# Kernel tuning notes

Hardware: AMD Instinct MI355X
Metric: run time of the kernel (lower is better)

The kernel has to match this reference:

```python
import jax, jax.numpy as jnp
import numpy as np

B, L, D, H = 8, 1024, 1024, 16
DH = D // H  # dim_per_head = 64
HG = H // 2  # global/local head split


def setup_inputs() -> dict:
    key = jax.random.key(0)
    ks = jax.random.split(key, 10)
    s = 1.0 / np.sqrt(D)
    return {
        "key": jax.random.normal(ks[0], (B, L, D), jnp.float32),
        "value": jax.random.normal(ks[1], (B, L, D), jnp.float32),
        "query": jax.random.normal(ks[2], (B, L, D), jnp.float32),
        "mask": jax.random.bernoulli(ks[3], 0.1, (B, L, L)),
        "additional_mask": jax.random.bernoulli(ks[4], 0.1, (B, L)),
        "Wk": jax.random.normal(ks[5], (D, D), jnp.float32) * s,
        "bk": jnp.zeros((D,), jnp.float32),
        "Wv": jax.random.normal(ks[6], (D, D), jnp.float32) * s,
        "bv": jnp.zeros((D,), jnp.float32),
        "Wq": jax.random.normal(ks[7], (D, D), jnp.float32) * s,
        "bq": jnp.zeros((D,), jnp.float32),
        "Wo": jax.random.normal(ks[8], (D, D), jnp.float32) * s,
        "bo": jnp.zeros((D,), jnp.float32),
    }


def _shape(x):
    # [B, L, D] -> [B, H, L, DH]
    return x.reshape(B, -1, H, DH).transpose(0, 2, 1, 3)


def reference(key, value, query, mask, additional_mask,
              Wk, bk, Wv, bv, Wq, bq, Wo, bo):
    # projections (torch Linear: x @ W.T + b)
    k = _shape(key @ Wk.T + bk)
    v = _shape(value @ Wv.T + bv)
    q = _shape(query @ Wq.T + bq) * (1.0 / np.sqrt(DH))  # scale query (edge_feature=None, additional_mask given)

    qg, ql = q[:, :HG], q[:, HG:]
    kg, kl = k[:, :HG], k[:, HG:]
    vg, vl = v[:, :HG], v[:, HG:]

    # global heads: standard masked attention
    score_g = jnp.einsum('bhqd,bhkd->bhqk', qg, kg)
    top_score = score_g[:, 0]  # taken BEFORE masking, as in original
    score_g = jnp.where(mask[:, None, :, :], -1e18, score_g)
    attn_g = jax.nn.softmax(score_g, axis=-1)  # dropout = identity (eval)
    ctx_g = jnp.einsum('bhqk,bhkd->bhqd', attn_g, vg)

    # local heads: additional_mask [B, k] broadcast over heads and queries
    score_l = jnp.einsum('bhqd,bhkd->bhqk', ql, kl)
    score_l = jnp.where(additional_mask[:, None, None, :], -1e18, score_l)
    attn_l = jax.nn.softmax(score_l, axis=-1)
    ctx_l = jnp.einsum('bhqk,bhkd->bhqd', attn_l, vl)

    ctx = jnp.concatenate([ctx_g, ctx_l], axis=1)          # [B, H, L, DH]
    ctx = ctx.transpose(0, 2, 1, 3).reshape(B, -1, D)      # unshape -> [B, L, D]
    out = ctx @ Wo.T + bo
    return out, top_score
```

## Files before the change

kernel.cpp:

```cpp
#include <hip/hip_runtime.h>
#include <hip/hip_bf16.h>

typedef unsigned short u16;
typedef unsigned int u32;
typedef __attribute__((ext_vector_type(8))) short short8;
typedef __attribute__((ext_vector_type(4))) short short4v;
typedef __attribute__((ext_vector_type(4))) float floatx4;

#define BB 8
#define LL 1024
#define DD 1024
#define HH 16
#define DHH 64
#define NEGBIG (-3.0e38f)
#define QSCALE 0.1803368801111204f
#define LN2F   0.6931471805599453f
#define DEFER_THR 12.0f

__device__ inline u16 f2b(float f) {
  union { __hip_bfloat16 h; u16 u; } cv;
  cv.h = __float2bfloat16(f);
  return cv.u;
}
__device__ inline float b2f(u16 u) {
  union { u16 u; __hip_bfloat16 h; } cv;
  cv.u = u;
  return __bfloat162float(cv.h);
}
__device__ inline float fin(float v, float sentinel) {
  return (fabsf(v) < 1e30f) ? v : sentinel;
}
__device__ inline float fexp2(float x) {
#if __has_builtin(__builtin_amdgcn_exp2f)
  return __builtin_amdgcn_exp2f(x);
#else
  return exp2f(x);
#endif
}
__device__ inline void async16(const void* g, void* l) {
  __builtin_amdgcn_global_load_lds(
      (__attribute__((address_space(1))) void*)(const_cast<void*>(g)),
      (__attribute__((address_space(3))) void*)l, 16, 0, 0);
}


__global__ __launch_bounds__(256) void convpack(
    const float* __restrict__ Wk, const float* __restrict__ Wv,
    const float* __restrict__ Wq, const float* __restrict__ Wo,
    const int* __restrict__ mask, const int* __restrict__ amask,
    u16* __restrict__ Wkb, u16* __restrict__ Wvb, u16* __restrict__ Wqb,
    u16* __restrict__ Wob, u32* __restrict__ maskb, u32* __restrict__ amaskb) {
  const int job = blockIdx.y;
  const int gtid = blockIdx.x * 256 + threadIdx.x;
  const int stride = gridDim.x * 256;

  if (job < 4) {
    const float* src; u16* dst;
    switch (job) {
      case 0: src = Wk; dst = Wkb; break;
      case 1: src = Wv; dst = Wvb; break;
      case 2: src = Wq; dst = Wqb; break;
      default: src = Wo; dst = Wob; break;
    }
    const size_t n4 = (size_t)DD * DD / 4;
    for (size_t i = gtid; i < n4; i += stride) {
      float4 v = ((const float4*)src)[i];
      short4v s;
      s[0] = (short)f2b(v.x); s[1] = (short)f2b(v.y);
      s[2] = (short)f2b(v.z); s[3] = (short)f2b(v.w);
      *(short4v*)(dst + i * 4) = s;
    }
  } else if (job == 4) {
    const size_t nw = (size_t)BB * LL * LL / 32;
    for (size_t w = gtid; w < nw; w += stride) {
      const int4* src = (const int4*)(mask + w * 32);
      u32 bits = 0;
#pragma unroll
      for (int c = 0; c < 8; c++) {
        int4 v = src[c];
        bits |= (u32)(v.x != 0) << (c * 4);
        bits |= (u32)(v.y != 0) << (c * 4 + 1);
        bits |= (u32)(v.z != 0) << (c * 4 + 2);
        bits |= (u32)(v.w != 0) << (c * 4 + 3);
      }
      maskb[w] = bits;
    }
  } else {
    const int nw = BB * LL / 32;
    for (int w = gtid; w < nw; w += stride) {
      const int4* src = (const int4*)(amask + w * 32);
      u32 bits = 0;
#pragma unroll
      for (int c = 0; c < 8; c++) {
        int4 v = src[c];
        bits |= (u32)(v.x != 0) << (c * 4);
        bits |= (u32)(v.y != 0) << (c * 4 + 1);
        bits |= (u32)(v.z != 0) << (c * 4 + 2);
        bits |= (u32)(v.w != 0) << (c * 4 + 3);
      }
      amaskb[w] = bits;
    }
  }
}

__global__ __launch_bounds__(256) void gemm_qkv(
    const float* __restrict__ key, const float* __restrict__ value,
    const float* __restrict__ query, const u16* __restrict__ Wkb,
    const u16* __restrict__ Wvb, const u16* __restrict__ Wqb,
    const float* __restrict__ bk, const float* __restrict__ bv,
    const float* __restrict__ bq, u16* __restrict__ kbuf,
    u16* __restrict__ vbt, u16* __restrict__ qbuf) {
  __shared__ u16 As[2][128 * 32];
  __shared__ u16 Ws[2][128 * 32];

  const int z = blockIdx.z;
  const int tid = threadIdx.x;
  const int wave = tid >> 6, lane = tid & 63;
  const int lr = lane & 15, lq = lane >> 4;
  const int row0 = blockIdx.x * 128;
  const int col0 = blockIdx.y * 128;
  const int wm = (wave & 1) * 64, wn = (wave >> 1) * 64;

  floatx4 acc[4][4];
#pragma unroll
  for (int i = 0; i < 4; i++)
#pragma unroll
    for (int j = 0; j < 4; j++) acc[i][j] = (floatx4){0.f, 0.f, 0.f, 0.f};

  const float* A = (z == 0) ? key : (z == 1) ? value : query;
  const u16* Wb  = (z == 0) ? Wkb : (z == 1) ? Wvb : Wqb;

  const int cc0 = tid, cc1 = 256 + tid;
  const u16* Wg0 = Wb + (size_t)(col0 + (cc0 >> 2)) * 1024 + (cc0 & 3) * 8;
  const u16* Wg1 = Wb + (size_t)(col0 + (cc1 >> 2)) * 1024 + (cc1 & 3) * 8;

  auto stageW = [&](int t, int buf) {
    const int o = t * 32;
    async16(Wg0 + o, &Ws[buf][wave * 512]);
    async16(Wg1 + o, &Ws[buf][2048 + wave * 512]);
  };
  auto loadA = [&](int t, float4* ag) {
#pragma unroll
    for (int it = 0; it < 4; it++) {
      const int cc = it * 256 + tid;
      ag[it] = *(const float4*)(A + (size_t)(row0 + (cc >> 3)) * 1024 +
                                (cc & 7) * 4 + t * 32);
    }
  };
  auto writeA = [&](int buf, const float4* ag) {
#pragma unroll
    for (int it = 0; it < 4; it++) {
      const int cc = it * 256 + tid;
      short4v s;
      s[0] = (short)f2b(ag[it].x); s[1] = (short)f2b(ag[it].y);
      s[2] = (short)f2b(ag[it].z); s[3] = (short)f2b(ag[it].w);
      *(short4v*)(&As[buf][(cc >> 3) * 32 + (cc & 7) * 4]) = s;
    }
  };

  {
    float4 ag0[4];
    loadA(0, ag0);
    stageW(0, 0);
    writeA(0, ag0);
  }

  for (int t = 0; t < 32; t++) {
    const int buf = t & 1;
    __syncthreads();
    float4 ag[4];
    if (t < 31) {
      stageW(t + 1, buf ^ 1);
      loadA(t + 1, ag);
    }

    short8 af[4], wf[4];
#pragma unroll
    for (int mi = 0; mi < 4; mi++)
      af[mi] = *(const short8*)(&As[buf][(wm + mi * 16 + lr) * 32 + lq * 8]);
#pragma unroll
    for (int ni = 0; ni < 4; ni++)
      wf[ni] = *(const short8*)(&Ws[buf][(wn + ni * 16 + lr) * 32 + lq * 8]);
#pragma unroll
    for (int mi = 0; mi < 4; mi++)
#pragma unroll
      for (int ni = 0; ni < 4; ni++)
        acc[mi][ni] = __builtin_amdgcn_mfma_f32_16x16x32_bf16(af[mi], wf[ni],
                                                              acc[mi][ni], 0, 0, 0);

    if (t < 31) writeA(buf ^ 1, ag);
  }

  const float scale = (z == 2) ? QSCALE : 1.0f;
  const float* bias = (z == 0) ? bk : (z == 1) ? bv : bq;
  u16* outb = (z == 0) ? kbuf : qbuf;

#pragma unroll
  for (int ni = 0; ni < 4; ni++) {
    const int col = col0 + wn + ni * 16 + lr;
    const float bvv = bias[col];
#pragma unroll
    for (int mi = 0; mi < 4; mi++) {
#pragma unroll
      for (int r = 0; r < 4; r++) {
        const int row = row0 + wm + mi * 16 + lq * 4 + r;
        const float v = (acc[mi][ni][r] + bvv) * scale;
        const int b = row >> 10, l = row & 1023, h = col >> 6, dh = col & 63;
        if (z == 1)
          vbt[((b * HH + h) * DHH + dh) * LL + l] = f2b(v);
        else
          outb[((b * HH + h) * LL + l) * DHH + dh] = f2b(v);
      }
    }
  }
}

template <int OUT>
__global__ __launch_bounds__(256) void gemm_b(
    const u16* __restrict__ A, const u16* __restrict__ Wb,
    const float* __restrict__ bias, void* __restrict__ outv, float scale) {
  __shared__ u16 As[128 * 32];
  __shared__ u16 Ws[128 * 32];

  const int tid = threadIdx.x;
  const int wave = tid >> 6, lane = tid & 63;
  const int lr = lane & 15, lq = lane >> 4;
  const int row0 = blockIdx.x * 128;
  const int col0 = blockIdx.y * 128;
  const int wm = (wave & 1) * 64, wn = (wave >> 1) * 64;

  floatx4 acc[4][4];
#pragma unroll
  for (int i = 0; i < 4; i++)
#pragma unroll
    for (int j = 0; j < 4; j++) acc[i][j] = (floatx4){0.f, 0.f, 0.f, 0.f};

  const int cc0 = tid, cc1 = 256 + tid;
  const u16* Ag0 = A + (size_t)(row0 + (cc0 >> 2)) * 1024 + (cc0 & 3) * 8;
  const u16* Ag1 = A + (size_t)(row0 + (cc1 >> 2)) * 1024 + (cc1 & 3) * 8;
  const u16* Wg0 = Wb + (size_t)(col0 + (cc0 >> 2)) * 1024 + (cc0 & 3) * 8;
  const u16* Wg1 = Wb + (size_t)(col0 + (cc1 >> 2)) * 1024 + (cc1 & 3) * 8;
  u16* As0 = As + wave * 512;
  u16* As1 = As + 2048 + wave * 512;
  u16* Ws0 = Ws + wave * 512;
  u16* Ws1 = Ws + 2048 + wave * 512;

  for (int k0 = 0; k0 < 1024; k0 += 32) {
    __syncthreads();
    async16(Ag0 + k0, As0);
    async16(Ag1 + k0, As1);
    async16(Wg0 + k0, Ws0);
    async16(Wg1 + k0, Ws1);
    __syncthreads();

    short8 af[4], wf[4];
#pragma unroll
    for (int mi = 0; mi < 4; mi++)
      af[mi] = *(const short8*)(As + (wm + mi * 16 + lr) * 32 + lq * 8);
#pragma unroll
    for (int ni = 0; ni < 4; ni++)
      wf[ni] = *(const short8*)(Ws + (wn + ni * 16 + lr) * 32 + lq * 8);
#pragma unroll
    for (int mi = 0; mi < 4; mi++)
#pragma unroll
      for (int ni = 0; ni < 4; ni++)
        acc[mi][ni] = __builtin_amdgcn_mfma_f32_16x16x32_bf16(af[mi], wf[ni],
                                                              acc[mi][ni], 0, 0, 0);
  }

#pragma unroll
  for (int ni = 0; ni < 4; ni++) {
    const int col = col0 + wn + ni * 16 + lr;
    const float bv = bias[col];
#pragma unroll
    for (int mi = 0; mi < 4; mi++) {
#pragma unroll
      for (int r = 0; r < 4; r++) {
        const int row = row0 + wm + mi * 16 + lq * 4 + r;
        const float v = (acc[mi][ni][r] + bv) * scale;
        if (OUT == 0) {
          const int b = row >> 10, l = row & 1023, h = col >> 6, dh = col & 63;
          ((u16*)outv)[((b * HH + h) * LL + l) * DHH + dh] = f2b(v);
        } else if (OUT == 2) {
          const int b = row >> 10, l = row & 1023, h = col >> 6, dh = col & 63;
          ((u16*)outv)[((b * HH + h) * DHH + dh) * LL + l] = f2b(v);
        } else {
          ((float*)outv)[(size_t)row * 1024 + col] = v;
        }
      }
    }
  }
}

__global__ __launch_bounds__(256) void attn_fast(
    const u16* __restrict__ qbuf, const u16* __restrict__ kbuf,
    const u16* __restrict__ vbt, const u32* __restrict__ maskb,
    const u32* __restrict__ amaskb, u16* __restrict__ ctx,
    float* __restrict__ top) {
  __shared__ u16 Ks[2][64 * 64];
  __shared__ u16 Vts[2][64 * 64];

  const int id = blockIdx.x;
  const int xcd = id & 7;
  const int r_ = id >> 3;
  const int b = r_ & 7;
  const int h = (((r_ >> 3) & 1) << 3) | (xcd ^ b);
  const int qt = r_ >> 4;

  const int tid = threadIdx.x, wave = tid >> 6, lane = tid & 63;
  const int lr = lane & 15, lq = lane >> 4;
  const int lq4 = lq * 4;
  const int x7 = lr & 7;

  const u16* Qg = qbuf + (size_t)((b * HH + h) * LL + qt * 128) * DHH;
  const u16* Kg = kbuf + (size_t)((b * HH + h) * LL) * DHH;
  const u16* Vtg = vbt + (size_t)((b * HH + h) * DHH) * LL;

  short8 qf[2][2];
#pragma unroll
  for (int mi = 0; mi < 2; mi++)
#pragma unroll
    for (int kk = 0; kk < 2; kk++)
      qf[mi][kk] = *(const short8*)(Qg + (wave * 32 + mi * 16 + lr) * 64 +
                                    kk * 32 + lq * 8);

  const int g0 = tid, g1 = 256 + tid;
  const int kr0 = g0 >> 3, kc0 = (g0 & 7) ^ (kr0 & 7);
  const int kr1 = g1 >> 3, kc1 = (g1 & 7) ^ (kr1 & 7);
  const int cs0 = ((0 + lq) ^ x7) * 8;
  const int cs1 = ((4 + lq) ^ x7) * 8;
  const int lqh = lq >> 1, lqb = (lq & 1) * 4;
  const int go00 = ((0 + lqh) ^ x7) * 8 + lqb;
  const int go01 = ((2 + lqh) ^ x7) * 8 + lqb;
  const int go10 = ((4 + lqh) ^ x7) * 8 + lqb;
  const int go11 = ((6 + lqh) ^ x7) * 8 + lqb;

  auto stage = [&](int kc, int buf) {
    async16(Kg + kc * 4096 + kr0 * 64 + kc0 * 8, &Ks[buf][wave * 512]);
    async16(Kg + kc * 4096 + kr1 * 64 + kc1 * 8, &Ks[buf][2048 + wave * 512]);
    async16(Vtg + (size_t)kr0 * LL + kc * 64 + kc0 * 8, &Vts[buf][wave * 512]);
    async16(Vtg + (size_t)kr1 * LL + kc * 64 + kc1 * 8,
            &Vts[buf][2048 + wave * 512]);
  };

  const int rowm0 = qt * 128 + wave * 32 + lr;
  const int rowm1 = rowm0 + 16;
  const u32* mb0 = (h < 8) ? maskb + (size_t)(b * LL + rowm0) * 32
                           : amaskb + b * 32;
  const u32* mb1 = (h < 8) ? maskb + (size_t)(b * LL + rowm1) * 32
                           : amaskb + b * 32;
  uint2 mwc0 = *(const uint2*)(mb0);
  uint2 mwc1 = *(const uint2*)(mb1);

  float mrow[2], lrow[2];
  floatx4 Oacc[2][4];
#pragma unroll
  for (int mi = 0; mi < 2; mi++) {
    mrow[mi] = NEGBIG;
    lrow[mi] = 0.f;
#pragma unroll
    for (int ni = 0; ni < 4; ni++) Oacc[mi][ni] = (floatx4){0.f, 0.f, 0.f, 0.f};
  }

  stage(0, 0);

  for (int kc = 0; kc < 16; kc++) {
    const int cur = kc & 1;
    __syncthreads();
    uint2 mwn0, mwn1;
    if (kc < 15) {
      stage(kc + 1, cur ^ 1);
      mwn0 = *(const uint2*)(mb0 + (kc + 1) * 2);
      mwn1 = *(const uint2*)(mb1 + (kc + 1) * 2);
    }
    const u16* Ksc = Ks[cur];
    const u16* Vtsc = Vts[cur];

    floatx4 S[2][4];
    __builtin_amdgcn_s_setprio(1);
#pragma unroll
    for (int nj = 0; nj < 4; nj++) {
      const short8 kf0 = *(const short8*)(Ksc + (nj * 16 + lr) * 64 + cs0);
      const short8 kf1 = *(const short8*)(Ksc + (nj * 16 + lr) * 64 + cs1);
#pragma unroll
      for (int mi = 0; mi < 2; mi++) {
        floatx4 z = (floatx4){0.f, 0.f, 0.f, 0.f};
        z = __builtin_amdgcn_mfma_f32_16x16x32_bf16(kf1, qf[mi][1], z, 0, 0, 0);
        z = __builtin_amdgcn_mfma_f32_16x16x32_bf16(kf0, qf[mi][0], z, 0, 0, 0);
        S[mi][nj] = z;
      }
    }
    __builtin_amdgcn_s_setprio(0);

    short8 pf[2][2];
#pragma unroll
    for (int mi = 0; mi < 2; mi++) {
      const int row = qt * 128 + wave * 32 + mi * 16 + lr;

      if (h == 0) {
        float* tp = top + (size_t)(b * LL + row) * LL + kc * 64 + lq4;
#pragma unroll
        for (int nj = 0; nj < 4; nj++) {
          float4 t;
          t.x = S[mi][nj][0] * LN2F; t.y = S[mi][nj][1] * LN2F;
          t.z = S[mi][nj][2] * LN2F; t.w = S[mi][nj][3] * LN2F;
          *(float4*)(tp + nj * 16) = t;
        }
      }

      {
        const uint2 mw = mi ? mwc1 : mwc0;
#pragma unroll
        for (int nj = 0; nj < 4; nj++) {
          const u32 nib = (((nj & 2) ? mw.y : mw.x) >> ((nj & 1) * 16 + lq4)) & 15u;
#pragma unroll
          for (int r = 0; r < 4; r++)
            if ((nib >> r) & 1) S[mi][nj][r] = -1e18f;
        }
      }

      float cm = fmaxf(fmaxf(S[mi][0][0], S[mi][0][1]),
                       fmaxf(S[mi][0][2], S[mi][0][3]));
#pragma unroll
      for (int nj = 1; nj < 4; nj++)
        cm = fmaxf(cm, fmaxf(fmaxf(S[mi][nj][0], S[mi][nj][1]),
                             fmaxf(S[mi][nj][2], S[mi][nj][3])));
      cm = fmaxf(cm, __shfl_xor(cm, 16, 64));
      cm = fmaxf(cm, __shfl_xor(cm, 32, 64));
      const float mold = mrow[mi];
      if (!__all(cm <= mold + DEFER_THR)) {
        const float mnew = fmaxf(mold, cm);
        const float alpha = fexp2(mold - mnew);
        mrow[mi] = mnew;
        lrow[mi] *= alpha;
#pragma unroll
        for (int ni = 0; ni < 4; ni++)
#pragma unroll
          for (int r = 0; r < 4; r++) Oacc[mi][ni][r] *= alpha;
      }
      const float mcur = mrow[mi];
      float rs = 0.f;
#pragma unroll
      for (int nj = 0; nj < 4; nj++)
#pragma unroll
        for (int r = 0; r < 4; r++) {
          const float p = fexp2(S[mi][nj][r] - mcur);
          S[mi][nj][r] = p;
          rs += p;
        }
      rs += __shfl_xor(rs, 16, 64);
      rs += __shfl_xor(rs, 32, 64);
      lrow[mi] += rs;

#pragma unroll
      for (int kk = 0; kk < 2; kk++) {
        short8 p;
#pragma unroll
        for (int r = 0; r < 4; r++) {
          p[r] = (short)f2b(S[mi][2 * kk][r]);
          p[4 + r] = (short)f2b(S[mi][2 * kk + 1][r]);
        }
        pf[mi][kk] = p;
      }
    }

    __builtin_amdgcn_s_setprio(1);
#pragma unroll
    for (int ni = 0; ni < 4; ni++) {
      const int rb = (ni * 16 + lr) * 64;
      const short4v v00 = *(const short4v*)(Vtsc + rb + go00);
      const short4v v01 = *(const short4v*)(Vtsc + rb + go01);
      const short4v v10 = *(const short4v*)(Vtsc + rb + go10);
      const short4v v11 = *(const short4v*)(Vtsc + rb + go11);
      const short8 vf0 = __builtin_shufflevector(v00, v01, 0, 1, 2, 3, 4, 5, 6, 7);
      const short8 vf1 = __builtin_shufflevector(v10, v11, 0, 1, 2, 3, 4, 5, 6, 7);
#pragma unroll
      for (int mi = 0; mi < 2; mi++) {
        Oacc[mi][ni] =
            __builtin_amdgcn_mfma_f32_16x16x32_bf16(vf0, pf[mi][0], Oacc[mi][ni], 0, 0, 0);
        Oacc[mi][ni] =
            __builtin_amdgcn_mfma_f32_16x16x32_bf16(vf1, pf[mi][1], Oacc[mi][ni], 0, 0, 0);
      }
    }
    __builtin_amdgcn_s_setprio(0);

    if (kc < 15) { mwc0 = mwn0; mwc1 = mwn1; }
  }

#pragma unroll
  for (int mi = 0; mi < 2; mi++) {
    const float inv = 1.0f / lrow[mi];
    const int row = qt * 128 + wave * 32 + mi * 16 + lr;
    u16* cp = ctx + (size_t)(b * LL + row) * DD + h * DHH + lq4;
#pragma unroll
    for (int ni = 0; ni < 4; ni++) {
      short4v o;
      o[0] = (short)f2b(Oacc[mi][ni][0] * inv);
      o[1] = (short)f2b(Oacc[mi][ni][1] * inv);
      o[2] = (short)f2b(Oacc[mi][ni][2] * inv);
      o[3] = (short)f2b(Oacc[mi][ni][3] * inv);
      *(short4v*)(cp + ni * 16) = o;
    }
  }
}

template <int MODE>
__global__ __launch_bounds__(256) void gemm_k(
    const void* __restrict__ Av, const float* __restrict__ W,
    const float* __restrict__ biasp, void* __restrict__ outv, float scale) {
  __shared__ u16 As[128 * 32];
  __shared__ u16 Ws[128 * 32];
  const int tid = threadIdx.x;
  const int wave = tid >> 6, lane = tid & 63;
  const int lr = lane & 15, lq = lane >> 4;
  const int row0 = blockIdx.x * 128;
  const int col0 = blockIdx.y * 128;
  const int wm = (wave & 1) * 64, wn = (wave >> 1) * 64;
  floatx4 acc[4][4];
#pragma unroll
  for (int i = 0; i < 4; i++)
#pragma unroll
    for (int j = 0; j < 4; j++) acc[i][j] = (floatx4){0.f, 0.f, 0.f, 0.f};
  const float* Af = (const float*)Av;
  const u16* Ab = (const u16*)Av;
  for (int k0 = 0; k0 < 1024; k0 += 32) {
    float4 wg[4];
#pragma unroll
    for (int it = 0; it < 4; it++) {
      const int cc = it * 256 + tid;
      wg[it] = *(const float4*)(W + (size_t)(col0 + (cc >> 3)) * 1024 + (cc & 7) * 4 + k0);
    }
    float4 ag[4];
    short8 ab0, ab1;
    if (MODE == 0) {
#pragma unroll
      for (int it = 0; it < 4; it++) {
        const int cc = it * 256 + tid;
        ag[it] = *(const float4*)(Af + (size_t)(row0 + (cc >> 3)) * 1024 + (cc & 7) * 4 + k0);
      }
    } else {
      const int cc0 = tid, cc1 = 256 + tid;
      ab0 = *(const short8*)(Ab + (size_t)(row0 + (cc0 >> 2)) * 1024 + (cc0 & 3) * 8 + k0);
      ab1 = *(const short8*)(Ab + (size_t)(row0 + (cc1 >> 2)) * 1024 + (cc1 & 3) * 8 + k0);
    }
    __syncthreads();
#pragma unroll
    for (int it = 0; it < 4; it++) {
      const int cc = it * 256 + tid;
      short4v s;
      s[0] = (short)f2b(wg[it].x); s[1] = (short)f2b(wg[it].y);
      s[2] = (short)f2b(wg[it].z); s[3] = (short)f2b(wg[it].w);
      *(short4v*)(Ws + (cc >> 3) * 32 + (cc & 7) * 4) = s;
    }
    if (MODE == 0) {
#pragma unroll
      for (int it = 0; it < 4; it++) {
        const int cc = it * 256 + tid;
        short4v s;
        s[0] = (short)f2b(ag[it].x); s[1] = (short)f2b(ag[it].y);
        s[2] = (short)f2b(ag[it].z); s[3] = (short)f2b(ag[it].w);
        *(short4v*)(As + (cc >> 3) * 32 + (cc & 7) * 4) = s;
      }
    } else {
      *(short8*)(As + tid * 8) = ab0;
      *(short8*)(As + (256 + tid) * 8) = ab1;
    }
    __syncthreads();
    short8 af[4], wf[4];
#pragma unroll
    for (int mi = 0; mi < 4; mi++)
      af[mi] = *(const short8*)(As + (wm + mi * 16 + lr) * 32 + lq * 8);
#pragma unroll
    for (int ni = 0; ni < 4; ni++)
      wf[ni] = *(const short8*)(Ws + (wn + ni * 16 + lr) * 32 + lq * 8);
#pragma unroll
    for (int mi = 0; mi < 4; mi++)
#pragma unroll
      for (int ni = 0; ni < 4; ni++)
        acc[mi][ni] = __builtin_amdgcn_mfma_f32_16x16x32_bf16(af[mi], wf[ni], acc[mi][ni], 0, 0, 0);
  }
#pragma unroll
  for (int ni = 0; ni < 4; ni++) {
    const int col = col0 + wn + ni * 16 + lr;
    const float bv = biasp[col];
#pragma unroll
    for (int mi = 0; mi < 4; mi++) {
#pragma unroll
      for (int r = 0; r < 4; r++) {
        const int row = row0 + wm + mi * 16 + lq * 4 + r;
        float v = (acc[mi][ni][r] + bv) * scale;
        v = fin(v, MODE == 0 ? 700.0f : 1000.0f);
        if (MODE == 0) {
          const int b = row >> 10, l = row & 1023, h = col >> 6, dh = col & 63;
          ((u16*)outv)[((b * HH + h) * LL + l) * DHH + dh] = f2b(v);
        } else {
          ((float*)outv)[(size_t)row * 1024 + col] = v;
        }
      }
    }
  }
}

__global__ __launch_bounds__(256) void attn_kernel(
    const u16* __restrict__ qbuf, const u16* __restrict__ kbuf,
    const u16* __restrict__ vbuf, const int* __restrict__ mask,
    const int* __restrict__ amask, u16* __restrict__ ctx,
    float* __restrict__ top) {
  __shared__ u16 Qs[128 * 64];
  __shared__ u16 Ks[64 * 64];
  __shared__ u16 Vts[64 * 64];
  __shared__ u16 Ps[4][32 * 64];
  const int qt = blockIdx.x, h = blockIdx.y, b = blockIdx.z;
  const int tid = threadIdx.x, wave = tid >> 6, lane = tid & 63;
  const int lr = lane & 15, lq = lane >> 4;
  const u16* Qg = qbuf + (size_t)((b * HH + h) * LL + qt * 128) * DHH;
  const u16* Kg = kbuf + (size_t)((b * HH + h) * LL) * DHH;
  const u16* Vg = vbuf + (size_t)((b * HH + h) * LL) * DHH;
#pragma unroll
  for (int it = 0; it < 4; it++) {
    short8 qv = *(const short8*)(Qg + (it * 256 + tid) * 8);
    *(short8*)(Qs + (it * 256 + tid) * 8) = qv;
  }
  float mrow[2][4], lrow[2][4];
  floatx4 Oacc[2][4];
#pragma unroll
  for (int mi = 0; mi < 2; mi++)
#pragma unroll
    for (int r = 0; r < 4; r++) { mrow[mi][r] = NEGBIG; lrow[mi][r] = 0.f; }
#pragma unroll
  for (int mi = 0; mi < 2; mi++)
#pragma unroll
    for (int ni = 0; ni < 4; ni++) Oacc[mi][ni] = (floatx4){0.f, 0.f, 0.f, 0.f};
  for (int kc = 0; kc < 16; kc++) {
    const u16* Kc = Kg + kc * 64 * DHH;
    const u16* Vc = Vg + kc * 64 * DHH;
    short8 kv0 = *(const short8*)(Kc + tid * 8);
    short8 kv1 = *(const short8*)(Kc + (256 + tid) * 8);
    short8 vv0 = *(const short8*)(Vc + tid * 8);
    short8 vv1 = *(const short8*)(Vc + (256 + tid) * 8);
    __syncthreads();
    *(short8*)(Ks + tid * 8) = kv0;
    *(short8*)(Ks + (256 + tid) * 8) = kv1;
    {
      const int r0 = tid >> 3, e0 = (tid & 7) * 8;
#pragma unroll
      for (int j = 0; j < 8; j++) Vts[(e0 + j) * 64 + r0] = (u16)vv0[j];
      const int cc1 = 256 + tid;
      const int r1 = cc1 >> 3, e1 = (cc1 & 7) * 8;
#pragma unroll
      for (int j = 0; j < 8; j++) Vts[(e1 + j) * 64 + r1] = (u16)vv1[j];
    }
    __syncthreads();
    floatx4 S[2][4];
    short8 qf[2][2];
#pragma unroll
    for (int mi = 0; mi < 2; mi++)
#pragma unroll
      for (int kk = 0; kk < 2; kk++)
        qf[mi][kk] = *(const short8*)(Qs + (wave * 32 + mi * 16 + lr) * 64 + kk * 32 + lq * 8);
#pragma unroll
    for (int nj = 0; nj < 4; nj++) {
      short8 kf0 = *(const short8*)(Ks + (nj * 16 + lr) * 64 + lq * 8);
      short8 kf1 = *(const short8*)(Ks + (nj * 16 + lr) * 64 + 32 + lq * 8);
#pragma unroll
      for (int mi = 0; mi < 2; mi++) {
        floatx4 z = (floatx4){0.f, 0.f, 0.f, 0.f};
        z = __builtin_amdgcn_mfma_f32_16x16x32_bf16(qf[mi][1], kf1, z, 0, 0, 0);
        z = __builtin_amdgcn_mfma_f32_16x16x32_bf16(qf[mi][0], kf0, z, 0, 0, 0);
        S[mi][nj] = z;
      }
    }
#pragma unroll
    for (int mi = 0; mi < 2; mi++)
#pragma unroll
      for (int nj = 0; nj < 4; nj++)
#pragma unroll
        for (int r = 0; r < 4; r++) S[mi][nj][r] = fin(S[mi][nj][r], 800.0f);
    if (h == 0) {
#pragma unroll
      for (int mi = 0; mi < 2; mi++)
#pragma unroll
        for (int nj = 0; nj < 4; nj++)
#pragma unroll
          for (int r = 0; r < 4; r++) {
            const int row = qt * 128 + wave * 32 + mi * 16 + lq * 4 + r;
            const int colk = kc * 64 + nj * 16 + lr;
            top[(size_t)(b * LL + row) * LL + colk] = S[mi][nj][r];
          }
    }
    if (h < 8) {
#pragma unroll
      for (int mi = 0; mi < 2; mi++)
#pragma unroll
        for (int r = 0; r < 4; r++) {
          const int row = qt * 128 + wave * 32 + mi * 16 + lq * 4 + r;
          const int* mp = mask + (size_t)(b * LL + row) * LL + kc * 64;
#pragma unroll
          for (int nj = 0; nj < 4; nj++) {
            const int mv = mp[nj * 16 + lr];
            S[mi][nj][r] = mv ? -1e18f : S[mi][nj][r];
          }
        }
    } else {
#pragma unroll
      for (int nj = 0; nj < 4; nj++) {
        const int mv = amask[b * LL + kc * 64 + nj * 16 + lr];
        if (mv) {
#pragma unroll
          for (int mi = 0; mi < 2; mi++)
#pragma unroll
            for (int r = 0; r < 4; r++) S[mi][nj][r] = -1e18f;
        }
      }
    }
#pragma unroll
    for (int mi = 0; mi < 2; mi++) {
#pragma unroll
      for (int r = 0; r < 4; r++) {
        float cm = S[mi][0][r];
#pragma unroll
        for (int nj = 1; nj < 4; nj++) cm = fmaxf(cm, S[mi][nj][r]);
#pragma unroll
        for (int off = 1; off < 16; off <<= 1) cm = fmaxf(cm, __shfl_xor(cm, off, 64));
        const float mold = mrow[mi][r];
        const float mnew = fmaxf(mold, cm);
        const float alpha = __expf(mold - mnew);
        mrow[mi][r] = mnew;
        float rs = 0.f;
#pragma unroll
        for (int nj = 0; nj < 4; nj++) {
          const float p = __expf(S[mi][nj][r] - mnew);
          S[mi][nj][r] = p;
          rs += p;
        }
#pragma unroll
        for (int off = 1; off < 16; off <<= 1) rs += __shfl_xor(rs, off, 64);
        lrow[mi][r] = lrow[mi][r] * alpha + rs;
#pragma unroll
        for (int ni = 0; ni < 4; ni++) Oacc[mi][ni][r] *= alpha;
      }
    }
#pragma unroll
    for (int mi = 0; mi < 2; mi++)
#pragma unroll
      for (int nj = 0; nj < 4; nj++)
#pragma unroll
        for (int r = 0; r < 4; r++)
          Ps[wave][(mi * 16 + lq * 4 + r) * 64 + nj * 16 + lr] = f2b(S[mi][nj][r]);
    __syncthreads();
#pragma unroll
    for (int kk = 0; kk < 2; kk++) {
      short8 pf[2];
#pragma unroll
      for (int mi = 0; mi < 2; mi++)
        pf[mi] = *(const short8*)(&Ps[wave][(mi * 16 + lr) * 64 + kk * 32 + lq * 8]);
#pragma unroll
      for (int ni = 0; ni < 4; ni++) {
        short8 vf = *(const short8*)(Vts + (ni * 16 + lr) * 64 + kk * 32 + lq * 8);
#pragma unroll
        for (int mi = 0; mi < 2; mi++)
          Oacc[mi][ni] = __builtin_amdgcn_mfma_f32_16x16x32_bf16(pf[mi], vf, Oacc[mi][ni], 0, 0, 0);
      }
    }
  }
#pragma unroll
  for (int mi = 0; mi < 2; mi++)
#pragma unroll
    for (int r = 0; r < 4; r++) {
      const float inv = 1.0f / lrow[mi][r];
      const int row = qt * 128 + wave * 32 + mi * 16 + lq * 4 + r;
#pragma unroll
      for (int ni = 0; ni < 4; ni++) {
        const int col = h * DHH + ni * 16 + lr;
        ctx[(size_t)(b * LL + row) * DD + col] = f2b(fin(Oacc[mi][ni][r] * inv, 900.0f));
      }
    }
}

extern "C" void kernel_launch(void* const* d_in, const int* in_sizes, int n_in,
                              void* d_out, int out_size, void* d_ws, size_t ws_size,
                              hipStream_t stream) {
  const float* key   = (const float*)d_in[0];
  const float* value = (const float*)d_in[1];
  const float* query = (const float*)d_in[2];
  const int* mask    = (const int*)d_in[3];
  const int* amask   = (const int*)d_in[4];
  const float* Wk = (const float*)d_in[5];
  const float* bk = (const float*)d_in[6];
  const float* Wv = (const float*)d_in[7];
  const float* bv = (const float*)d_in[8];
  const float* Wq = (const float*)d_in[9];
  const float* bq = (const float*)d_in[10];
  const float* Wo = (const float*)d_in[11];
  const float* bo = (const float*)d_in[12];

  float* outp = (float*)d_out;
  float* topp = outp + (size_t)BB * LL * DD;

  const size_t M8 = (size_t)BB * LL * DD;
  const size_t M1 = (size_t)DD * DD;
  const size_t NEED = (size_t)90 * 1024 * 1024;

  dim3 tb(256), gg(64, 8, 1), ga(8, 16, 8);

  if (ws_size >= NEED) {
    u16* W16 = (u16*)d_ws;
    u16* Wkb = W16;
    u16* Wvb = Wkb + M1;
    u16* Wqb = Wvb + M1;
    u16* Wob = Wqb + M1;
    u32* maskb = (u32*)(Wob + M1);
    u32* amaskb = maskb + 262144;
    u16* kbuf = W16 + 6 * M1;
    u16* vbt  = kbuf + M8;
    u16* qbuf = vbt + M8;
    u16* cbuf = qbuf + M8;

    convpack<<<dim3(256, 6), tb, 0, stream>>>(
        Wk, Wv, Wq, Wo, mask, amask, Wkb, Wvb, Wqb, Wob, maskb, amaskb);
    gemm_qkv<<<dim3(64, 8, 3), tb, 0, stream>>>(
        key, value, query, Wkb, Wvb, Wqb, bk, bv, bq, kbuf, vbt, qbuf);
    attn_fast<<<dim3(1024, 1, 1), tb, 0, stream>>>(qbuf, kbuf, vbt, maskb,
                                                   amaskb, cbuf, topp);
    gemm_b<1><<<gg, tb, 0, stream>>>(cbuf, Wob, bo, outp, 1.0f);
  } else {
    u16* kbuf = (u16*)d_ws;
    u16* vbuf = kbuf + M8;
    u16* qbuf = vbuf + M8;
    u16* cbuf = qbuf + M8;
    gemm_k<0><<<gg, tb, 0, stream>>>(key,   Wk, bk, kbuf, 1.0f);
    gemm_k<0><<<gg, tb, 0, stream>>>(value, Wv, bv, vbuf, 1.0f);
    gemm_k<0><<<gg, tb, 0, stream>>>(query, Wq, bq, qbuf, 0.125f);
    attn_kernel<<<ga, tb, 0, stream>>>(qbuf, kbuf, vbuf, mask, amask, cbuf, topp);
    gemm_k<1><<<gg, tb, 0, stream>>>(cbuf, Wo, bo, outp, 1.0f);
  }
}
```

Baseline: 412.9 us.

## Triple-buffer GEMM shared-memory stages with explicit vmcnt waits

Both GEMM kernels (QKV projection and the bf16 GEMM used for the output projection) move from single or double buffering to a three-stage shared-memory ring. Global loads now run two to three k-steps ahead, governed by explicit s_waitcnt vmcnt counts and raw s_barrier calls in place of __syncthreads. The aim is to hide global-memory latency behind the MFMA work and to drop the second barrier per iteration in gemm_b. In exchange it uses more LDS and registers, which may lower occupancy. The hand-counted vmcnt values are fragile, and the tail iterations re-load clamped tiles, adding redundant traffic.

Result: faster. 388.8 us (-5.8%).

```diff
diff --git a/kernel.cpp b/kernel.cpp
--- a/kernel.cpp
+++ b/kernel.cpp
@@ -111,7 +111,7 @@
     const float* __restrict__ bq, u16* __restrict__ kbuf,
     u16* __restrict__ vbt, u16* __restrict__ qbuf) {
   __shared__ u16 As[2][128 * 32];
-  __shared__ u16 Ws[2][128 * 32];
+  __shared__ u16 Ws[3][128 * 32];
 
   const int z = blockIdx.z;
   const int tid = threadIdx.x;
@@ -134,10 +134,10 @@
   const u16* Wg0 = Wb + (size_t)(col0 + (cc0 >> 2)) * 1024 + (cc0 & 3) * 8;
   const u16* Wg1 = Wb + (size_t)(col0 + (cc1 >> 2)) * 1024 + (cc1 & 3) * 8;
 
-  auto stageW = [&](int t, int buf) {
+  auto stageW = [&](int t, int wbuf) {
     const int o = t * 32;
-    async16(Wg0 + o, &Ws[buf][wave * 512]);
-    async16(Wg1 + o, &Ws[buf][2048 + wave * 512]);
+    async16(Wg0 + o, &Ws[wbuf][wave * 512]);
+    async16(Wg1 + o, &Ws[wbuf][2048 + wave * 512]);
   };
   auto loadA = [&](int t, float4* ag) {
 #pragma unroll
@@ -147,40 +147,47 @@
                                 (cc & 7) * 4 + t * 32);
     }
   };
-  auto writeA = [&](int buf, const float4* ag) {
+  auto writeA = [&](int abuf, const float4* ag) {
 #pragma unroll
     for (int it = 0; it < 4; it++) {
       const int cc = it * 256 + tid;
       short4v s;
       s[0] = (short)f2b(ag[it].x); s[1] = (short)f2b(ag[it].y);
       s[2] = (short)f2b(ag[it].z); s[3] = (short)f2b(ag[it].w);
-      *(short4v*)(&As[buf][(cc >> 3) * 32 + (cc & 7) * 4]) = s;
+      *(short4v*)(&As[abuf][(cc >> 3) * 32 + (cc & 7) * 4]) = s;
     }
   };
 
-  {
-    float4 ag0[4];
-    loadA(0, ag0);
-    stageW(0, 0);
-    writeA(0, ag0);
-  }
-
+  float4 ag[3][4];
+
+  stageW(0, 0);
+  stageW(1, 1);
+  loadA(0, ag[0]);
+  loadA(1, ag[1]);
+  asm volatile("s_waitcnt vmcnt(4)" ::: "memory");
+  writeA(0, ag[0]);
+  loadA(2, ag[2]);
+
+#pragma unroll
   for (int t = 0; t < 32; t++) {
-    const int buf = t & 1;
-    __syncthreads();
-    float4 ag[4];
-    if (t < 31) {
-      stageW(t + 1, buf ^ 1);
-      loadA(t + 1, ag);
-    }
+    const int abuf = t & 1;
+    asm volatile("s_waitcnt vmcnt(10)" ::: "memory");
+    asm volatile("s_waitcnt lgkmcnt(0)" ::: "memory");
+    __builtin_amdgcn_s_barrier();
+    asm volatile("" ::: "memory");
+
+    const int t2 = (t + 2 < 32) ? t + 2 : 31;
+    const int t3 = (t + 3 < 32) ? t + 3 : 31;
+    stageW(t2, (t + 2) % 3);
+    loadA(t3, ag[t % 3]);
 
     short8 af[4], wf[4];
 #pragma unroll
     for (int mi = 0; mi < 4; mi++)
-      af[mi] = *(const short8*)(&As[buf][(wm + mi * 16 + lr) * 32 + lq * 8]);
+      af[mi] = *(const short8*)(&As[abuf][(wm + mi * 16 + lr) * 32 + lq * 8]);
 #pragma unroll
     for (int ni = 0; ni < 4; ni++)
-      wf[ni] = *(const short8*)(&Ws[buf][(wn + ni * 16 + lr) * 32 + lq * 8]);
+      wf[ni] = *(const short8*)(&Ws[t % 3][(wn + ni * 16 + lr) * 32 + lq * 8]);
 #pragma unroll
     for (int mi = 0; mi < 4; mi++)
 #pragma unroll
@@ -188,7 +195,9 @@
         acc[mi][ni] = __builtin_amdgcn_mfma_f32_16x16x32_bf16(af[mi], wf[ni],
                                                               acc[mi][ni], 0, 0, 0);
 
-    if (t < 31) writeA(buf ^ 1, ag);
+    if (t == 0) asm volatile("s_waitcnt vmcnt(10)" ::: "memory");
+    else        asm volatile("s_waitcnt vmcnt(12)" ::: "memory");
+    writeA(abuf ^ 1, ag[(t + 1) % 3]);
   }
 
   const float scale = (z == 2) ? QSCALE : 1.0f;
@@ -219,8 +228,8 @@
 __global__ __launch_bounds__(256) void gemm_b(
     const u16* __restrict__ A, const u16* __restrict__ Wb,
     const float* __restrict__ bias, void* __restrict__ outv, float scale) {
-  __shared__ u16 As[128 * 32];
-  __shared__ u16 Ws[128 * 32];
+  __shared__ u16 As[3][128 * 32];
+  __shared__ u16 Ws[3][128 * 32];
 
   const int tid = threadIdx.x;
   const int wave = tid >> 6, lane = tid & 63;
@@ -240,26 +249,34 @@
   const u16* Ag1 = A + (size_t)(row0 + (cc1 >> 2)) * 1024 + (cc1 & 3) * 8;
   const u16* Wg0 = Wb + (size_t)(col0 + (cc0 >> 2)) * 1024 + (cc0 & 3) * 8;
   const u16* Wg1 = Wb + (size_t)(col0 + (cc1 >> 2)) * 1024 + (cc1 & 3) * 8;
-  u16* As0 = As + wave * 512;
-  u16* As1 = As + 2048 + wave * 512;
-  u16* Ws0 = Ws + wave * 512;
-  u16* Ws1 = Ws + 2048 + wave * 512;
-
-  for (int k0 = 0; k0 < 1024; k0 += 32) {
-    __syncthreads();
-    async16(Ag0 + k0, As0);
-    async16(Ag1 + k0, As1);
-    async16(Wg0 + k0, Ws0);
-    async16(Wg1 + k0, Ws1);
-    __syncthreads();
+
+  auto stage = [&](int t, int buf) {
+    const int o = t * 32;
+    async16(Ag0 + o, &As[buf][wave * 512]);
+    async16(Ag1 + o, &As[buf][2048 + wave * 512]);
+    async16(Wg0 + o, &Ws[buf][wave * 512]);
+    async16(Wg1 + o, &Ws[buf][2048 + wave * 512]);
+  };
+
+  stage(0, 0);
+  stage(1, 1);
+
+#pragma unroll
+  for (int t = 0; t < 32; t++) {
+    asm volatile("s_waitcnt vmcnt(4)" ::: "memory");
+    __builtin_amdgcn_s_barrier();
+    asm volatile("" ::: "memory");
+
+    const int t2 = (t + 2 < 32) ? t + 2 : 31;
+    stage(t2, (t + 2) % 3);
 
     short8 af[4], wf[4];
 #pragma unroll
     for (int mi = 0; mi < 4; mi++)
-      af[mi] = *(const short8*)(As + (wm + mi * 16 + lr) * 32 + lq * 8);
+      af[mi] = *(const short8*)(&As[t % 3][(wm + mi * 16 + lr) * 32 + lq * 8]);
 #pragma unroll
     for (int ni = 0; ni < 4; ni++)
-      wf[ni] = *(const short8*)(Ws + (wn + ni * 16 + lr) * 32 + lq * 8);
+      wf[ni] = *(const short8*)(&Ws[t % 3][(wn + ni * 16 + lr) * 32 + lq * 8]);
 #pragma unroll
     for (int mi = 0; mi < 4; mi++)
 #pragma unroll
```
